# Kernel tuning notes

Hardware: AMD Instinct MI355X
Metric: run time of the kernel (lower is better)

Reference implementation:

```python
import jax, jax.numpy as jnp
import numpy as np

B, CIN, H, W = 8, 64, 128, 128
COUT, K = 64, 3
STRIDE, PAD, DIL, G = 1, 1, 1, 1
T = K * K
HO = (H + 2 * PAD - (DIL * (K - 1) + 1)) // STRIDE + 1
WO = (W + 2 * PAD - (DIL * (K - 1) + 1)) // STRIDE + 1


def setup_inputs() -> dict:
    key = jax.random.key(0)
    ks = jax.random.split(key, 5)
    x = jax.random.normal(ks[0], (B, CIN, H, W), jnp.float32)
    offset = jax.random.normal(ks[1], (B, 2 * G * T, HO, WO), jnp.float32)
    mask = jax.random.uniform(ks[2], (B, G * T, HO, WO), jnp.float32)
    weight = jax.random.normal(ks[3], (COUT, CIN, K, K), jnp.float32) * (1.0 / np.sqrt(CIN * T))
    bias = jnp.zeros((COUT,), jnp.float32)
    return {"x": x, "offset": offset, "mask": mask, "weight": weight, "bias": bias}


def _gather(img_f, idx):
    # img_f: [Cg, H*W], idx: [T, Ho, Wo] -> [Cg, T, Ho, Wo]
    return img_f[:, idx]


def _dcn(x, offset, mask, weight, bias):
    Bn, Cin, Hh, Ww = x.shape
    Cout = weight.shape[0]
    Cg = Cin // G
    # offset channels laid out as [G, T, (dy, dx)] per DCNv2 convention
    off = offset.reshape(Bn, G, T, 2, HO, WO)
    dy, dx = off[:, :, :, 0], off[:, :, :, 1]  # [B, G, T, Ho, Wo]
    ky, kx = jnp.meshgrid(jnp.arange(K), jnp.arange(K), indexing="ij")
    ky = (ky.reshape(T) * DIL).astype(jnp.float32)
    kx = (kx.reshape(T) * DIL).astype(jnp.float32)
    base_y = (jnp.arange(HO) * STRIDE - PAD).astype(jnp.float32)
    base_x = (jnp.arange(WO) * STRIDE - PAD).astype(jnp.float32)
    # absolute sampling coordinates per (batch, def-group, tap, out-row, out-col)
    py = dy + base_y[None, None, None, :, None] + ky[None, None, :, None, None]
    px = dx + base_x[None, None, None, None, :] + kx[None, None, :, None, None]
    y0 = jnp.floor(py)
    x0 = jnp.floor(px)
    imgf = x.reshape(Bn, G, Cg, Hh * Ww)
    gather = jax.vmap(jax.vmap(_gather))  # over B and G
    sampled = jnp.zeros((Bn, G, Cg, T, HO, WO), x.dtype)
    # bilinear interpolation with zero padding outside the image
    for oy, ox in ((y0, x0), (y0, x0 + 1.0), (y0 + 1.0, x0), (y0 + 1.0, x0 + 1.0)):
        wgt = (1.0 - jnp.abs(py - oy)) * (1.0 - jnp.abs(px - ox))
        valid = (oy >= 0) & (oy < Hh) & (ox >= 0) & (ox < Ww)
        yi = jnp.clip(oy, 0, Hh - 1).astype(jnp.int32)
        xi = jnp.clip(ox, 0, Ww - 1).astype(jnp.int32)
        vals = gather(imgf, yi * Ww + xi)  # [B, G, Cg, T, Ho, Wo]
        sampled = sampled + vals * (wgt * valid)[:, :, None]
    # modulation mask, then accumulate taps into output channels
    m = mask.reshape(Bn, G, T, HO, WO)
    sampled = sampled * m[:, :, None]
    wr = weight.reshape(Cout, G, Cg, T)
    out = jnp.einsum("bgctij,ogct->boij", sampled, wr) + bias[None, :, None, None]
    return out


def reference(x, offset, mask, weight, bias):
    return _dcn(x, offset, mask, weight, bias)
```

## Files before the change

kernel.cpp:

```cpp
#include <hip/hip_runtime.h>
#include <stdint.h>

#define Bn   8
#define CIN  64
#define Hh   128
#define Wh   128
#define COUT 64
#define Tt   9
#define HO   128
#define WO   128
#define HW   (HO * WO)

#define RH     15
#define RWC    25
#define RREC   (RH * RWC)
#define RSTR   144
#define HALO_Y 3
#define HALO_X 4

typedef _Float16 h16;
typedef __attribute__((ext_vector_type(2)))  _Float16 h2;
typedef __attribute__((ext_vector_type(8)))  _Float16 h8;
typedef __attribute__((ext_vector_type(16))) float    f16v;

__device__ h16 g_xT[(size_t)Bn * Hh * Wh * CIN];
__device__ h16 g_wh[Tt * 4 * 2 * 64 * 8];

__global__ __launch_bounds__(256) void prep(const float* __restrict__ x,
                                            const float* __restrict__ w) {
    if (blockIdx.x >= Bn * Hh) {
        int tid = (blockIdx.x - Bn * Hh) * 256 + threadIdx.x;
        int t   = tid >> 12;
        int rem = tid & 4095;
        int ks  = rem >> 10;
        int mt  = (rem >> 9) & 1;
        int ln  = (rem >> 3) & 63;
        int j   = rem & 7;
        int o   = mt * 32 + (ln & 31);
        int c   = ks * 16 + ((ln >> 5) << 3) + j;
        g_wh[tid] = (h16)w[(size_t)(o * 64 + c) * 9 + t];
        return;
    }
    int b = blockIdx.x >> 7;
    int y = blockIdx.x & 127;
    __shared__ uint32_t tile[64][65];

    const float* src = x + ((size_t)b * CIN) * (Hh * Wh) + (size_t)y * Wh;
    int t    = threadIdx.x;
    int xp   = t & 63;
    int csub = t >> 6;
    #pragma unroll
    for (int cc = 0; cc < 64; cc += 4) {
        int c = cc + csub;
        float2 v = *(const float2*)(src + (size_t)c * (Hh * Wh) + xp * 2);
        uint32_t h0 = (uint32_t)__builtin_bit_cast(uint16_t, (h16)v.x);
        uint32_t h1 = (uint32_t)__builtin_bit_cast(uint16_t, (h16)v.y);
        tile[c][xp] = h0 | (h1 << 16);
    }
    __syncthreads();

    uint32_t* dst = (uint32_t*)(g_xT + (((size_t)b * Hh + y) * Wh) * CIN);
    int d  = t & 31;
    int xo = t >> 5;
    #pragma unroll
    for (int it = 0; it < 16; ++it) {
        int xg = it * 8 + xo;
        uint32_t lo = tile[2 * d][xg >> 1];
        uint32_t hi = tile[2 * d + 1][xg >> 1];
        int sh = (xg & 1) * 16;
        uint32_t l0 = (lo >> sh) & 0xffffu;
        uint32_t h1 = (hi >> sh) & 0xffffu;
        dst[xg * 32 + d] = l0 | (h1 << 16);
    }
}

__global__ __launch_bounds__(256) void dcn_main(
        const float* __restrict__ offset, const float* __restrict__ mask,
        const float* __restrict__ bias, float* __restrict__ out) {
    __shared__ __align__(16) uint8_t sreg[RREC * RSTR];

    int blk  = blockIdx.x;
    int b    = blk & 7;
    int s    = blk >> 3;
    int ty   = s >> 3, tx = s & 7;
    int i0   = ty * 8, j0 = tx * 16;
    int lane = threadIdx.x & 63;
    int wave = threadIdx.x >> 6;
    int n    = lane & 31;
    int g    = lane >> 5;

    const h16* xb = g_xT + (size_t)b * (Hh * Wh * CIN);

    int i = i0 + 2 * wave + (n >> 4);
    int j = j0 + (n & 15);
    int p = (i << 7) + j;

    const float* offB = offset + (size_t)b * (2 * Tt * HW);
    const float* mskB = mask   + (size_t)b * (Tt * HW);
    float dyv[Tt], dxv[Tt], mmv[Tt];
    #pragma unroll
    for (int t = 0; t < Tt; ++t) {
        dyv[t] = offB[(2 * t) * HW + p];
        dxv[t] = offB[(2 * t + 1) * HW + p];
        mmv[t] = mskB[t * HW + p];
    }

    {
        const int base_y = i0 - HALO_Y, base_x = j0 - HALO_X;
        #pragma unroll
        for (int it = 0; it < 12; ++it) {
            int idx  = it * 256 + threadIdx.x;
            int rec  = idx >> 3;
            int quad = idx & 7;
            if (rec < RREC) {
                int ry = rec / RWC, rx = rec - ry * RWC;
                int gy = min(max(base_y + ry, 0), Hh - 1);
                int gx = min(max(base_x + rx, 0), Wh - 1);
                uint4 v = *(const uint4*)(xb + ((gy << 7) + gx) * 64 + quad * 8);
                *(uint4*)(sreg + rec * RSTR + quad * 16) = v;
            }
        }
    }
    __syncthreads();

    f16v acc[2] = {};

    #pragma unroll
    for (int t = 0; t < Tt; ++t) {
        const int ky = t / 3, kx = t % 3;
        float py = dyv[t] + (float)(i + ky - 1);
        float px = dxv[t] + (float)(j + kx - 1);
        float fy = floorf(py), fx = floorf(px);
        int   y0 = (int)fy,    x0 = (int)fx;
        float ly = py - fy,    lx = px - fx;
        float hy = 1.f - ly,   hx = 1.f - lx;
        float m = mmv[t];
        hy *= m; ly *= m;

        bool vy0 = (y0 >= 0) && (y0 < Hh);
        bool vy1 = (y0 >= -1) && (y0 < Hh - 1);
        bool vx0 = (x0 >= 0) && (x0 < Wh);
        bool vx1 = (x0 >= -1) && (x0 < Wh - 1);
        float w00 = (vy0 && vx0) ? hy * hx : 0.f;
        float w01 = (vy0 && vx1) ? hy * lx : 0.f;
        float w10 = (vy1 && vx0) ? ly * hx : 0.f;
        float w11 = (vy1 && vx1) ? ly * lx : 0.f;

        int ry = y0 - i0 + HALO_Y;
        int rx = x0 - j0 + HALO_X;
        bool intile = (ry >= 0) & (ry <= RH - 2) & (rx >= 0) & (rx <= RWC - 2);
        int ryc = min(max(ry, 0), RH - 2), rxc = min(max(rx, 0), RWC - 2);
        int pl00 = ryc * RWC + rxc;
        const uint8_t* cbase = sreg + pl00 * RSTR + g * 16;

        union U4 { uint4 v; h2 h[4]; };
        U4 c00[4], c01[4], c10[4], c11[4];
        #pragma unroll
        for (int ks = 0; ks < 4; ++ks) {
            c00[ks].v = *(const uint4*)(cbase + ks * 32);
            c01[ks].v = *(const uint4*)(cbase + RSTR + ks * 32);
            c10[ks].v = *(const uint4*)(cbase + RWC * RSTR + ks * 32);
            c11[ks].v = *(const uint4*)(cbase + (RWC + 1) * RSTR + ks * 32);
        }
        if (__any(!intile)) {
            if (!intile) {
                int y0c = min(max(y0, 0), Hh - 1), y1c = min(max(y0 + 1, 0), Hh - 1);
                int x0c = min(max(x0, 0), Wh - 1), x1c = min(max(x0 + 1, 0), Wh - 1);
                const h16* r0 = xb + (size_t)(y0c * Wh) * CIN;
                const h16* r1 = xb + (size_t)(y1c * Wh) * CIN;
                #pragma unroll
                for (int ks = 0; ks < 4; ++ks) {
                    int c = ks * 16 + g * 8;
                    c00[ks].v = *(const uint4*)(r0 + x0c * CIN + c);
                    c01[ks].v = *(const uint4*)(r0 + x1c * CIN + c);
                    c10[ks].v = *(const uint4*)(r1 + x0c * CIN + c);
                    c11[ks].v = *(const uint4*)(r1 + x1c * CIN + c);
                }
            }
        }

        h2 W00 = {(h16)w00, (h16)w00};
        h2 W01 = {(h16)w01, (h16)w01};
        h2 W10 = {(h16)w10, (h16)w10};
        h2 W11 = {(h16)w11, (h16)w11};

        const h16* wt = g_wh + t * 4096;
        #pragma unroll
        for (int ks = 0; ks < 4; ++ks) {
            union { h2 r[4]; h8 v; } pk;
            #pragma unroll
            for (int e = 0; e < 4; ++e) {
                h2 r = c00[ks].h[e] * W00;
                r = c01[ks].h[e] * W01 + r;
                r = c10[ks].h[e] * W10 + r;
                r = c11[ks].h[e] * W11 + r;
                pk.r[e] = r;
            }
            #pragma unroll
            for (int mt = 0; mt < 2; ++mt) {
                h8 a = *(const h8*)(wt + (ks * 2 + mt) * 512 + lane * 8);
                acc[mt] = __builtin_amdgcn_mfma_f32_32x32x16_f16(
                    a, pk.v, acc[mt], 0, 0, 0);
            }
        }
    }

    #pragma unroll
    for (int mt = 0; mt < 2; ++mt) {
        #pragma unroll
        for (int r = 0; r < 16; ++r) {
            int o = mt * 32 + (r & 3) + 8 * (r >> 2) + 4 * g;
            out[(size_t)(b * COUT + o) * HW + p] = acc[mt][r] + bias[o];
        }
    }
}

extern "C" void kernel_launch(void* const* d_in, const int* in_sizes, int n_in,
                              void* d_out, int out_size, void* d_ws, size_t ws_size,
                              hipStream_t stream) {
    const float* x      = (const float*)d_in[0];
    const float* offset = (const float*)d_in[1];
    const float* mask   = (const float*)d_in[2];
    const float* weight = (const float*)d_in[3];
    const float* bias   = (const float*)d_in[4];
    (void)d_ws; (void)ws_size;

    prep<<<Bn * Hh + 144, 256, 0, stream>>>(x, weight);
    dcn_main<<<Bn * 128, 256, 0, stream>>>(offset, mask, bias, (float*)d_out);
}
```

Measured before the change: 126.7 us.

## Enlarge LDS halo and move out-of-tile gathers to deferred correction pass

Grows the shared-memory input region vertically (halo 4 rows, 17 rows total) so fewer sampling points fall outside the tile. Out-of-tile taps no longer load from global memory inside the main loop; their weights are zeroed, they are recorded in a bitmask, and a separate pass after the main loop recomputes and gathers them, issuing extra MFMAs only for waves that contain such lanes. This keeps the hot loop branch-free and LDS-only, at the cost of a larger LDS tile (lower occupancy headroom), more staging loads, and duplicated coordinate math plus extra MFMAs in the fallback pass.

```diff
diff --git a/kernel.cpp b/kernel.cpp
--- a/kernel.cpp
+++ b/kernel.cpp
@@ -11,11 +11,11 @@
 #define WO   128
 #define HW   (HO * WO)
 
-#define RH     15
+#define RH     17
 #define RWC    25
 #define RREC   (RH * RWC)
 #define RSTR   144
-#define HALO_Y 3
+#define HALO_Y 4
 #define HALO_X 4
 
 typedef _Float16 h16;
@@ -108,7 +108,7 @@
     {
         const int base_y = i0 - HALO_Y, base_x = j0 - HALO_X;
         #pragma unroll
-        for (int it = 0; it < 12; ++it) {
+        for (int it = 0; it < 14; ++it) {
             int idx  = it * 256 + threadIdx.x;
             int rec  = idx >> 3;
             int quad = idx & 7;
@@ -124,6 +124,7 @@
     __syncthreads();
 
     f16v acc[2] = {};
+    unsigned fbmask = 0;
 
     #pragma unroll
     for (int t = 0; t < Tt; ++t) {
@@ -141,14 +142,19 @@
         bool vy1 = (y0 >= -1) && (y0 < Hh - 1);
         bool vx0 = (x0 >= 0) && (x0 < Wh);
         bool vx1 = (x0 >= -1) && (x0 < Wh - 1);
+
+        int ry = y0 - i0 + HALO_Y;
+        int rx = x0 - j0 + HALO_X;
+        bool intile = (ry >= 0) & (ry <= RH - 2) & (rx >= 0) & (rx <= RWC - 2);
+        fbmask |= intile ? 0u : (1u << t);
+        float keep = intile ? 1.f : 0.f;
+        hx *= keep; lx *= keep;
+
         float w00 = (vy0 && vx0) ? hy * hx : 0.f;
         float w01 = (vy0 && vx1) ? hy * lx : 0.f;
         float w10 = (vy1 && vx0) ? ly * hx : 0.f;
         float w11 = (vy1 && vx1) ? ly * lx : 0.f;
 
-        int ry = y0 - i0 + HALO_Y;
-        int rx = x0 - j0 + HALO_X;
-        bool intile = (ry >= 0) & (ry <= RH - 2) & (rx >= 0) & (rx <= RWC - 2);
         int ryc = min(max(ry, 0), RH - 2), rxc = min(max(rx, 0), RWC - 2);
         int pl00 = ryc * RWC + rxc;
         const uint8_t* cbase = sreg + pl00 * RSTR + g * 16;
@@ -161,22 +167,6 @@
             c01[ks].v = *(const uint4*)(cbase + RSTR + ks * 32);
             c10[ks].v = *(const uint4*)(cbase + RWC * RSTR + ks * 32);
             c11[ks].v = *(const uint4*)(cbase + (RWC + 1) * RSTR + ks * 32);
-        }
-        if (__any(!intile)) {
-            if (!intile) {
-                int y0c = min(max(y0, 0), Hh - 1), y1c = min(max(y0 + 1, 0), Hh - 1);
-                int x0c = min(max(x0, 0), Wh - 1), x1c = min(max(x0 + 1, 0), Wh - 1);
-                const h16* r0 = xb + (size_t)(y0c * Wh) * CIN;
-                const h16* r1 = xb + (size_t)(y1c * Wh) * CIN;
-                #pragma unroll
-                for (int ks = 0; ks < 4; ++ks) {
-                    int c = ks * 16 + g * 8;
-                    c00[ks].v = *(const uint4*)(r0 + x0c * CIN + c);
-                    c01[ks].v = *(const uint4*)(r0 + x1c * CIN + c);
-                    c10[ks].v = *(const uint4*)(r1 + x0c * CIN + c);
-                    c11[ks].v = *(const uint4*)(r1 + x1c * CIN + c);
-                }
-            }
         }
 
         h2 W00 = {(h16)w00, (h16)w00};
@@ -206,6 +196,70 @@
     }
 
     #pragma unroll
+    for (int t = 0; t < Tt; ++t) {
+        if (__any((fbmask >> t) & 1u)) {
+            h8 bf[4] = {};
+            if ((fbmask >> t) & 1u) {
+                const int ky = t / 3, kx = t % 3;
+                float py = dyv[t] + (float)(i + ky - 1);
+                float px = dxv[t] + (float)(j + kx - 1);
+                float fy = floorf(py), fx = floorf(px);
+                int   y0 = (int)fy,    x0 = (int)fx;
+                float ly = py - fy,    lx = px - fx;
+                float hy = 1.f - ly,   hx = 1.f - lx;
+                float m = mmv[t];
+                hy *= m; ly *= m;
+                bool vy0 = (y0 >= 0) && (y0 < Hh);
+                bool vy1 = (y0 >= -1) && (y0 < Hh - 1);
+                bool vx0 = (x0 >= 0) && (x0 < Wh);
+                bool vx1 = (x0 >= -1) && (x0 < Wh - 1);
+                float w00 = (vy0 && vx0) ? hy * hx : 0.f;
+                float w01 = (vy0 && vx1) ? hy * lx : 0.f;
+                float w10 = (vy1 && vx0) ? ly * hx : 0.f;
+                float w11 = (vy1 && vx1) ? ly * lx : 0.f;
+                int y0c = min(max(y0, 0), Hh - 1), y1c = min(max(y0 + 1, 0), Hh - 1);
+                int x0c = min(max(x0, 0), Wh - 1), x1c = min(max(x0 + 1, 0), Wh - 1);
+                const h16* r0 = xb + (size_t)(y0c * Wh) * CIN;
+                const h16* r1 = xb + (size_t)(y1c * Wh) * CIN;
+                h2 W00 = {(h16)w00, (h16)w00};
+                h2 W01 = {(h16)w01, (h16)w01};
+                h2 W10 = {(h16)w10, (h16)w10};
+                h2 W11 = {(h16)w11, (h16)w11};
+                union U4 { uint4 v; h2 h[4]; };
+                #pragma unroll
+                for (int ks = 0; ks < 4; ++ks) {
+                    int c = ks * 16 + g * 8;
+                    U4 u00, u01, u10, u11;
+                    u00.v = *(const uint4*)(r0 + x0c * CIN + c);
+                    u01.v = *(const uint4*)(r0 + x1c * CIN + c);
+                    u10.v = *(const uint4*)(r1 + x0c * CIN + c);
+                    u11.v = *(const uint4*)(r1 + x1c * CIN + c);
+                    union { h2 r[4]; h8 v; } pk;
+                    #pragma unroll
+                    for (int e = 0; e < 4; ++e) {
+                        h2 r = u00.h[e] * W00;
+                        r = u01.h[e] * W01 + r;
+                        r = u10.h[e] * W10 + r;
+                        r = u11.h[e] * W11 + r;
+                        pk.r[e] = r;
+                    }
+                    bf[ks] = pk.v;
+                }
+            }
+            const h16* wt = g_wh + t * 4096;
+            #pragma unroll
+            for (int ks = 0; ks < 4; ++ks) {
+                #pragma unroll
+                for (int mt = 0; mt < 2; ++mt) {
+                    h8 a = *(const h8*)(wt + (ks * 2 + mt) * 512 + lane * 8);
+                    acc[mt] = __builtin_amdgcn_mfma_f32_32x32x16_f16(
+                        a, bf[ks], acc[mt], 0, 0, 0);
+                }
+            }
+        }
+    }
+
+    #pragma unroll
     for (int mt = 0; mt < 2; ++mt) {
         #pragma unroll
         for (int r = 0; r < 16; ++r) {
```

Measured after the change: 131.4 us. 3.8% more time.
